# Performance work log

Hardware: AMD Instinct MI355X
Metric: run time of the kernel (lower is better)

## Reference

```python
import jax, jax.numpy as jnp
import numpy as np

TOPK = 6
E = 512
IN = 384
M = 8192
LN_EPS = 1e-5


def _lin(x, w, b):
    # torch nn.Linear: y = x @ W^T + b, W is [out, in]
    return x @ w.T + b


def setup_inputs() -> dict:
    key = jax.random.key(0)
    ks = jax.random.split(key, 16)
    s = lambda k, sh: (jax.random.normal(k, sh, dtype=jnp.float32) * 0.02)
    return {
        "x": jax.random.normal(ks[0], (1, M, IN), dtype=jnp.float32),
        "fc1_w": s(ks[1], (E, IN)), "fc1_b": jnp.zeros((E,), jnp.float32),
        "wh_w": s(ks[2], (E, E)),   "wh_b": jnp.zeros((E,), jnp.float32),
        "wt_w": s(ks[3], (E, E)),   "wt_b": jnp.zeros((E,), jnp.float32),
        "l1_w": s(ks[4], (E, E)),   "l1_b": jnp.zeros((E,), jnp.float32),
        "l2_w": s(ks[5], (E, E)),   "l2_b": jnp.zeros((E,), jnp.float32),
        "a1_w": s(ks[6], (E // 2, E)), "a1_b": jnp.zeros((E // 2,), jnp.float32),
        "a2_w": s(ks[7], (1, E // 2)), "a2_b": jnp.zeros((1,), jnp.float32),
        "ln_g": jnp.ones((E,), jnp.float32), "ln_b": jnp.zeros((E,), jnp.float32),
    }


def reference(x, fc1_w, fc1_b, wh_w, wh_b, wt_w, wt_b,
              l1_w, l1_b, l2_w, l2_b, a1_w, a1_b, a2_w, a2_b, ln_g, ln_b):
    lrelu = jax.nn.leaky_relu  # slope 0.01 == torch default
    h = lrelu(_lin(x, fc1_w, fc1_b))                      # [B,M,E]
    h = (h + h.mean(axis=1, keepdims=True)) * 0.5
    e_h = _lin(h, wh_w, wh_b)                             # [B,M,E]
    e_t = _lin(h, wt_w, wt_b)                             # [B,M,E]
    scale = E ** (-0.5)
    attn_logit = (e_h * scale) @ jnp.swapaxes(e_t, -2, -1)  # [B,M,M]
    topk_weight, topk_index = jax.lax.top_k(attn_logit, TOPK)  # [B,M,K]
    # gather top-k neighbor tail embeddings: [B,M,K,E]
    Nb_h = jax.vmap(lambda et, idx: et[idx])(e_t, topk_index)
    topk_prob = jax.nn.softmax(topk_weight, axis=2)       # [B,M,K]
    eh_r = topk_prob[..., None] * Nb_h + (1.0 - topk_prob)[..., None] * e_h[:, :, None, :]
    gate = jnp.tanh(e_h[:, :, None, :] + eh_r)            # [B,M,K,E]
    # faithful to torch einsum('ijkl,ijkm->ijk'): sums l and m independently
    ka_weight = Nb_h.sum(axis=-1) * gate.sum(axis=-1)     # [B,M,K]
    ka_prob = jax.nn.softmax(ka_weight, axis=2)           # [B,M,K]
    e_Nh = jnp.einsum('bmk,bmke->bme', ka_prob, Nb_h)     # [B,M,E]
    sum_emb = lrelu(_lin(e_h + e_Nh, l1_w, l1_b))
    bi_emb = lrelu(_lin(e_h * e_Nh, l2_w, l2_b))
    emb = sum_emb + bi_emb                                # [B,M,E] (dropout = eval identity)
    hn = emb[0]                                           # squeeze(0) -> [M,E]
    # GeoGlobalAttention readout: gate_nn = Linear->LeakyReLU->Linear, softmax over nodes
    g = _lin(lrelu(_lin(hn, a1_w, a1_b)), a2_w, a2_b)     # [M,1]
    att = jax.nn.softmax(g, axis=0)
    pooled = (att * hn).sum(axis=0, keepdims=True)        # [1,E]
    mu = pooled.mean(axis=-1, keepdims=True)
    var = jnp.mean((pooled - mu) ** 2, axis=-1, keepdims=True)
    out = (pooled - mu) / jnp.sqrt(var + LN_EPS) * ln_g + ln_b
    return out
```

## Files before the change

kernel.cpp:

```cpp
#include <hip/hip_runtime.h>
#include <math.h>
#include <stdint.h>

#define M_NODES 8192
#define E_DIM   512
#define NTOPK   6
#define ATTN_SCALE 0.04419417382415922f

typedef __attribute__((ext_vector_type(8))) short short8;
typedef __attribute__((ext_vector_type(4))) float f32x4;

__device__ __forceinline__ float lrelu(float v) { return v > 0.f ? v : 0.01f * v; }

__device__ __forceinline__ unsigned short f2bf(float f) {
  uint32_t u = __float_as_uint(f);
  uint32_t r = (u + 0x7FFFu + ((u >> 16) & 1u)) >> 16;
  return (unsigned short)r;
}
__device__ __forceinline__ float bf2f(unsigned short s) {
  return __uint_as_float(((uint32_t)s) << 16);
}

__device__ __forceinline__ void async_cp16(const void* gptr, void* lds) {
  auto g1 = reinterpret_cast<const __attribute__((address_space(1))) unsigned int*>(
      reinterpret_cast<uintptr_t>(gptr));
  auto l3 = reinterpret_cast<__attribute__((address_space(3))) unsigned int*>(
      reinterpret_cast<uintptr_t>(lds));
  __builtin_amdgcn_global_load_lds(g1, l3, 16, 0, 0);
}



__global__ __launch_bounds__(256) void wcast_kernel(
    const float* __restrict__ x, const float* __restrict__ fc1w,
    const float* __restrict__ whw, const float* __restrict__ wtw,
    const float* __restrict__ l1w, const float* __restrict__ l2w,
    const float* __restrict__ a1w,
    unsigned short* __restrict__ xT, unsigned short* __restrict__ fc1T,
    unsigned short* __restrict__ whT, unsigned short* __restrict__ wtT,
    unsigned short* __restrict__ l1T, unsigned short* __restrict__ l2T,
    unsigned short* __restrict__ a1T)
{
  const int gid = blockIdx.x * 256 + threadIdx.x;
  const float* src; unsigned short* dst; int K8, local;
  if (gid < 417792) {
    K8 = 48;
    if (gid < 393216) { src = x; dst = xT; local = gid; }
    else { src = fc1w; dst = fc1T; local = gid - 393216; }
  } else {
    K8 = 64;
    if (gid < 450560)      { src = whw; dst = whT; local = gid - 417792; }
    else if (gid < 483328) { src = wtw; dst = wtT; local = gid - 450560; }
    else if (gid < 516096) { src = l1w; dst = l1T; local = gid - 483328; }
    else if (gid < 548864) { src = l2w; dst = l2T; local = gid - 516096; }
    else                   { src = a1w; dst = a1T; local = gid - 548864; }
  }
  const int m = local / K8;
  const int k8 = local - m * K8;
  const float* p = src + (size_t)m * (K8 * 8) + k8 * 8;
  float4 v0 = ((const float4*)p)[0];
  float4 v1 = ((const float4*)p)[1];
  const int Kt = K8 >> 2;
  const size_t ti = ((size_t)(m >> 4) * Kt + (k8 >> 2)) * 512 + ((m & 15) + 16 * (k8 & 3)) * 8;
  uint4 pk;
  pk.x = (uint32_t)f2bf(v0.x) | ((uint32_t)f2bf(v0.y) << 16);
  pk.y = (uint32_t)f2bf(v0.z) | ((uint32_t)f2bf(v0.w) << 16);
  pk.z = (uint32_t)f2bf(v1.x) | ((uint32_t)f2bf(v1.y) << 16);
  pk.w = (uint32_t)f2bf(v1.z) | ((uint32_t)f2bf(v1.w) << 16);
  *(uint4*)(dst + ti) = pk;
}

__global__ __launch_bounds__(256, 4) void gemm1_kernel(
    const unsigned short* __restrict__ xT, const unsigned short* __restrict__ fc1T,
    const float* __restrict__ b1, unsigned short* __restrict__ hT,
    float* __restrict__ colsum)
{
  __shared__ unsigned short As[8 * 512];
  __shared__ unsigned short Bs[8 * 512];
  const int tid = threadIdx.x, lane = tid & 63, w = tid >> 6;
  const int wr = w >> 1, wc = w & 1;
  const int m0 = blockIdx.y * 128;
  const int n0 = blockIdx.x * 128;

  f32x4 acc[4][4];
#pragma unroll
  for (int i = 0; i < 4; i++)
#pragma unroll
    for (int j = 0; j < 4; j++) acc[i][j] = (f32x4){0.f, 0.f, 0.f, 0.f};

  for (int kt = 0; kt < 12; kt++) {
    const int s0 = w, s1 = w + 4;
    async_cp16(xT + ((size_t)((m0 >> 4) + s0) * 12 + kt) * 512 + lane * 8, &As[s0 * 512]);
    async_cp16(xT + ((size_t)((m0 >> 4) + s1) * 12 + kt) * 512 + lane * 8, &As[s1 * 512]);
    async_cp16(fc1T + ((size_t)((n0 >> 4) + s0) * 12 + kt) * 512 + lane * 8, &Bs[s0 * 512]);
    async_cp16(fc1T + ((size_t)((n0 >> 4) + s1) * 12 + kt) * 512 + lane * 8, &Bs[s1 * 512]);
    __syncthreads();
    short8 a[4], b[4];
#pragma unroll
    for (int i = 0; i < 4; i++) a[i] = *(const short8*)&As[(wr * 4 + i) * 512 + lane * 8];
#pragma unroll
    for (int j = 0; j < 4; j++) b[j] = *(const short8*)&Bs[(wc * 4 + j) * 512 + lane * 8];
#pragma unroll
    for (int i = 0; i < 4; i++)
#pragma unroll
      for (int j = 0; j < 4; j++)
        acc[i][j] = __builtin_amdgcn_mfma_f32_16x16x32_bf16(a[i], b[j], acc[i][j], 0, 0, 0);
    __syncthreads();
  }

  const int q = lane >> 4, lcol = lane & 15;
  float colp[4] = {};
#pragma unroll
  for (int i = 0; i < 4; i++)
#pragma unroll
    for (int j = 0; j < 4; j++) {
      const int c = n0 + wc * 64 + j * 16 + lcol;
      const float bias = b1[c];
#pragma unroll
      for (int d = 0; d < 4; d++) {
        const int r = m0 + wr * 64 + i * 16 + q * 4 + d;
        const float v = 0.5f * lrelu(acc[i][j][d] + bias);
        hT[((size_t)(r >> 4) * 16 + (c >> 5)) * 512 +
           ((r & 15) + 16 * ((c >> 3) & 3)) * 8 + (c & 7)] = f2bf(v);
        colp[j] += v;
      }
    }
#pragma unroll
  for (int j = 0; j < 4; j++) {
    colp[j] += __shfl_xor(colp[j], 16);
    colp[j] += __shfl_xor(colp[j], 32);
  }
  if (lane < 16) {
#pragma unroll
    for (int j = 0; j < 4; j++)
      atomicAdd(&colsum[n0 + wc * 64 + j * 16 + lcol], colp[j]);
  }
}

__global__ __launch_bounds__(256) void meanproj_kernel(
    const float* __restrict__ colsum, const float* __restrict__ whw,
    const float* __restrict__ wtw, const float* __restrict__ whb,
    const float* __restrict__ wtb, float* __restrict__ biasHT)
{
  const int lane = threadIdx.x & 63;
  const int c1024 = blockIdx.x * 4 + (threadIdx.x >> 6);
  const bool isH = c1024 < 512;
  const int c = isH ? c1024 : c1024 - 512;
  const float* W = (isH ? whw : wtw) + (size_t)c * 512 + lane * 8;
  const float* cs = colsum + lane * 8;
  float s = 0.f;
#pragma unroll
  for (int e = 0; e < 8; e++) s = fmaf(cs[e], W[e], s);
#pragma unroll
  for (int off = 32; off; off >>= 1) s += __shfl_xor(s, off);
  if (lane == 0)
    biasHT[c1024] = (isH ? whb : wtb)[c] + s * (1.f / (float)M_NODES);
}

__global__ __launch_bounds__(256, 4) void dual_gemm(
    const unsigned short* __restrict__ hT, const unsigned short* __restrict__ wstackT,
    const float* __restrict__ biasHT,
    unsigned short* __restrict__ ehT, unsigned short* __restrict__ etT,
    unsigned short* __restrict__ ehRow, unsigned short* __restrict__ etRow)
{
  __shared__ unsigned short As[8 * 512];
  __shared__ unsigned short Bs[8 * 512];
  const int tid = threadIdx.x, lane = tid & 63, w = tid >> 6;
  const int wr = w >> 1, wc = w & 1;
  const int m0 = blockIdx.y * 128;
  const int n0 = blockIdx.x * 128;

  f32x4 acc[4][4];
#pragma unroll
  for (int i = 0; i < 4; i++)
#pragma unroll
    for (int j = 0; j < 4; j++) acc[i][j] = (f32x4){0.f, 0.f, 0.f, 0.f};

  for (int kt = 0; kt < 16; kt++) {
    const int s0 = w, s1 = w + 4;
    async_cp16(hT + ((size_t)((m0 >> 4) + s0) * 16 + kt) * 512 + lane * 8, &As[s0 * 512]);
    async_cp16(hT + ((size_t)((m0 >> 4) + s1) * 16 + kt) * 512 + lane * 8, &As[s1 * 512]);
    async_cp16(wstackT + ((size_t)((n0 >> 4) + s0) * 16 + kt) * 512 + lane * 8, &Bs[s0 * 512]);
    async_cp16(wstackT + ((size_t)((n0 >> 4) + s1) * 16 + kt) * 512 + lane * 8, &Bs[s1 * 512]);
    __syncthreads();
    short8 a[4], b[4];
#pragma unroll
    for (int i = 0; i < 4; i++) a[i] = *(const short8*)&As[(wr * 4 + i) * 512 + lane * 8];
#pragma unroll
    for (int j = 0; j < 4; j++) b[j] = *(const short8*)&Bs[(wc * 4 + j) * 512 + lane * 8];
#pragma unroll
    for (int i = 0; i < 4; i++)
#pragma unroll
      for (int j = 0; j < 4; j++)
        acc[i][j] = __builtin_amdgcn_mfma_f32_16x16x32_bf16(a[i], b[j], acc[i][j], 0, 0, 0);
    __syncthreads();
  }

  const int q = lane >> 4, lcol = lane & 15;
  const bool isH = (n0 < 512);
  const int cb = isH ? n0 : (n0 - 512);
  unsigned short* T = isH ? ehT : etT;
  unsigned short* R = isH ? ehRow : etRow;

#pragma unroll
  for (int i = 0; i < 4; i++)
#pragma unroll
    for (int j = 0; j < 4; j++) {
      const int cl = wc * 64 + j * 16 + lcol;
      const float bias = biasHT[n0 + cl];
      const int c = cb + cl;
#pragma unroll
      for (int d = 0; d < 4; d++) {
        const int r = m0 + wr * 64 + i * 16 + q * 4 + d;
        const unsigned short us = f2bf(acc[i][j][d] + bias);
        T[((size_t)(r >> 4) * 16 + (c >> 5)) * 512 +
          ((r & 15) + 16 * ((c >> 3) & 3)) * 8 + (c & 7)] = us;
        R[(size_t)r * E_DIM + c] = us;
      }
    }
}

template <int MODE>
__global__ __launch_bounds__(256) void mfma_gemm(
    const unsigned short* __restrict__ At1, const unsigned short* __restrict__ At2,
    const unsigned short* __restrict__ Wt1, const unsigned short* __restrict__ Wt2,
    const float* __restrict__ b1, const float* __restrict__ b2,
    float* __restrict__ Cf, unsigned short* __restrict__ T1,
    unsigned short* __restrict__ Cbf, int N, int K)
{
  constexpr bool DUALW = (MODE == 2);
  __shared__ unsigned short As[2][8 * 512];
  __shared__ unsigned short Bs[2][4 * 512];
  const int Kt = K >> 5;
  const int tid = threadIdx.x, lane = tid & 63, w = tid >> 6;
  const int m0 = blockIdx.y * 128, n0 = blockIdx.x * 64;

  f32x4 acc0[2][4], acc1[2][4];
#pragma unroll
  for (int p = 0; p < 2; p++)
#pragma unroll
    for (int j = 0; j < 4; j++) {
      acc0[p][j] = (f32x4){0.f, 0.f, 0.f, 0.f};
      acc1[p][j] = (f32x4){0.f, 0.f, 0.f, 0.f};
    }

  for (int kt = 0; kt < Kt; kt++) {
    const unsigned short* a1p = At1 + ((size_t)((m0 >> 4) + 2 * w) * Kt + kt) * 512 + lane * 8;
    async_cp16(a1p, &As[0][(2 * w) * 512]);
    async_cp16(a1p + (size_t)Kt * 512, &As[0][(2 * w + 1) * 512]);
    if (MODE == 2) {
      const unsigned short* a2p = At2 + ((size_t)((m0 >> 4) + 2 * w) * Kt + kt) * 512 + lane * 8;
      async_cp16(a2p, &As[1][(2 * w) * 512]);
      async_cp16(a2p + (size_t)Kt * 512, &As[1][(2 * w + 1) * 512]);
    }
    const unsigned short* bp1 = Wt1 + ((size_t)((n0 >> 4) + w) * Kt + kt) * 512 + lane * 8;
    async_cp16(bp1, &Bs[0][w * 512]);
    if (DUALW) {
      const unsigned short* bp2 = Wt2 + ((size_t)((n0 >> 4) + w) * Kt + kt) * 512 + lane * 8;
      async_cp16(bp2, &Bs[1][w * 512]);
    }
    __syncthreads();
    short8 a[2], a2[2], bb[4], bb2[4];
#pragma unroll
    for (int p = 0; p < 2; p++) a[p] = *(const short8*)&As[0][(2 * w + p) * 512 + lane * 8];
    if (MODE == 2) {
#pragma unroll
      for (int p = 0; p < 2; p++) a2[p] = *(const short8*)&As[1][(2 * w + p) * 512 + lane * 8];
    }
#pragma unroll
    for (int j = 0; j < 4; j++) bb[j] = *(const short8*)&Bs[0][j * 512 + lane * 8];
    if (DUALW) {
#pragma unroll
      for (int j = 0; j < 4; j++) bb2[j] = *(const short8*)&Bs[1][j * 512 + lane * 8];
    }
#pragma unroll
    for (int p = 0; p < 2; p++)
#pragma unroll
      for (int j = 0; j < 4; j++) {
        acc0[p][j] = __builtin_amdgcn_mfma_f32_16x16x32_bf16(a[p], bb[j], acc0[p][j], 0, 0, 0);
        if (MODE == 2)
          acc1[p][j] = __builtin_amdgcn_mfma_f32_16x16x32_bf16(a2[p], bb2[j], acc1[p][j], 0, 0, 0);
      }
    __syncthreads();
  }

  const int lrow = (lane >> 4) * 4, lcol = lane & 15;

  if (MODE == 3) {
    float part[2][4] = {};
#pragma unroll
    for (int p = 0; p < 2; p++)
#pragma unroll
      for (int j = 0; j < 4; j++) {
        const int c = n0 + j * 16 + lcol;
        const float bias1 = b1[c];
        const float w2 = b2[c];
#pragma unroll
        for (int d = 0; d < 4; d++)
          part[p][d] = fmaf(lrelu(acc0[p][j][d] + bias1), w2, part[p][d]);
      }
#pragma unroll
    for (int p = 0; p < 2; p++)
#pragma unroll
      for (int d = 0; d < 4; d++) {
#pragma unroll
        for (int off = 1; off < 16; off <<= 1)
          part[p][d] += __shfl_xor(part[p][d], off);
      }
    if (lcol == 0) {
#pragma unroll
      for (int p = 0; p < 2; p++)
#pragma unroll
        for (int d = 0; d < 4; d++)
          atomicAdd(&Cf[m0 + w * 32 + p * 16 + lrow + d], part[p][d]);
    }
    return;
  }

  const int NT = N >> 5;
#pragma unroll
  for (int p = 0; p < 2; p++)
#pragma unroll
    for (int j = 0; j < 4; j++) {
      const int c = n0 + j * 16 + lcol;
      const float bias1 = b1[c];
      const float bias2 = b2[c];
#pragma unroll
      for (int d = 0; d < 4; d++) {
        const int r = m0 + w * 32 + p * 16 + lrow + d;
        const float e = lrelu(acc0[p][j][d] + bias1) + lrelu(acc1[p][j][d] + bias2);
        T1[((size_t)(r >> 4) * NT + (c >> 5)) * 512 +
           ((r & 15) + 16 * ((c >> 3) & 3)) * 8 + (c & 7)] = f2bf(e);
        Cbf[(size_t)r * N + c] = f2bf(e);
      }
    }
}

__global__ __launch_bounds__(256, 4) void sgemm_kernel(
    const unsigned short* __restrict__ ehT, const unsigned short* __restrict__ etT,
    uint32_t* __restrict__ cand)
{
  __shared__ unsigned short SH[128 * 130];
  unsigned short* As = SH;
  unsigned short* Bs = SH + 4096;
  const int tid = threadIdx.x, lane = tid & 63, w = tid >> 6;
  const int wr = w >> 1, wc = w & 1;
  const int m0 = blockIdx.y * 128;
  const int n0 = blockIdx.x * 128;

  f32x4 acc[4][4];
#pragma unroll
  for (int i = 0; i < 4; i++)
#pragma unroll
    for (int j = 0; j < 4; j++) acc[i][j] = (f32x4){0.f, 0.f, 0.f, 0.f};

  for (int kt = 0; kt < 16; kt++) {
    const int s0 = w, s1 = w + 4;
    async_cp16(ehT + ((size_t)((m0 >> 4) + s0) * 16 + kt) * 512 + lane * 8, &As[s0 * 512]);
    async_cp16(ehT + ((size_t)((m0 >> 4) + s1) * 16 + kt) * 512 + lane * 8, &As[s1 * 512]);
    async_cp16(etT + ((size_t)((n0 >> 4) + s0) * 16 + kt) * 512 + lane * 8, &Bs[s0 * 512]);
    async_cp16(etT + ((size_t)((n0 >> 4) + s1) * 16 + kt) * 512 + lane * 8, &Bs[s1 * 512]);
    __syncthreads();
    short8 a[4], b[4];
#pragma unroll
    for (int i = 0; i < 4; i++) a[i] = *(const short8*)&As[(wr * 4 + i) * 512 + lane * 8];
#pragma unroll
    for (int j = 0; j < 4; j++) b[j] = *(const short8*)&Bs[(wc * 4 + j) * 512 + lane * 8];
#pragma unroll
    for (int i = 0; i < 4; i++)
#pragma unroll
      for (int j = 0; j < 4; j++)
        acc[i][j] = __builtin_amdgcn_mfma_f32_16x16x32_bf16(a[i], b[j], acc[i][j], 0, 0, 0);
    __syncthreads();
  }

  const int q = lane >> 4, lcol = lane & 15;

#pragma unroll
  for (int i = 0; i < 4; i++)
#pragma unroll
    for (int j = 0; j < 4; j++) {
      const int colb = wc * 64 + j * 16 + lcol;
#pragma unroll
      for (int d = 0; d < 4; d++)
        SH[(wr * 64 + i * 16 + q * 4 + d) * 130 + colb] = f2bf(acc[i][j][d]);
    }
  __syncthreads();

  const int r = tid >> 1, half = tid & 1;
  const uint32_t* rowp = (const uint32_t*)SH + r * 65 + half * 32;
  const int cbase = n0 + half * 64;
  uint32_t t0 = 0, t1 = 0, t2 = 0, t3 = 0, t4 = 0, t5 = 0;
#pragma unroll 4
  for (int cc = 0; cc < 32; cc++) {
    const uint32_t v = rowp[cc];
#pragma unroll
    for (int e = 0; e < 2; e++) {
      const uint32_t h = e ? (v >> 16) : (v & 0xFFFFu);
      const uint32_t o16 = (h & 0x8000u) ? ((~h) & 0xFFFFu) : (h | 0x8000u);
      const uint32_t k = (o16 << 16) | (uint32_t)(8191 - (cbase + 2 * cc + e));
      if (k > t5) {
        t5 = k;
        uint32_t tmp;
        if (t5 > t4) { tmp = t4; t4 = t5; t5 = tmp; }
        if (t4 > t3) { tmp = t3; t3 = t4; t4 = tmp; }
        if (t3 > t2) { tmp = t2; t2 = t3; t3 = tmp; }
        if (t2 > t1) { tmp = t1; t1 = t2; t2 = tmp; }
        if (t1 > t0) { tmp = t0; t0 = t1; t1 = tmp; }
      }
    }
  }

  uint32_t b0 = (uint32_t)__shfl_xor((int)t0, 1);
  uint32_t b1 = (uint32_t)__shfl_xor((int)t1, 1);
  uint32_t b2 = (uint32_t)__shfl_xor((int)t2, 1);
  uint32_t b3 = (uint32_t)__shfl_xor((int)t3, 1);
  uint32_t b4 = (uint32_t)__shfl_xor((int)t4, 1);
  uint32_t b5 = (uint32_t)__shfl_xor((int)t5, 1);
  uint32_t wk[6];
#pragma unroll
  for (int t = 0; t < 6; t++) {
    if (t0 > b0) {
      wk[t] = t0;
      t0 = t1; t1 = t2; t2 = t3; t3 = t4; t4 = t5; t5 = 0u;
    } else {
      wk[t] = b0;
      b0 = b1; b1 = b2; b2 = b3; b3 = b4; b4 = b5; b5 = 0u;
    }
  }

  if (half == 0) {
    uint32_t* cp = cand + ((size_t)blockIdx.x * M_NODES + m0 + r) * 6;
    uint2 p01; p01.x = wk[0]; p01.y = wk[1];
    uint2 p23; p23.x = wk[2]; p23.y = wk[3];
    uint2 p45; p45.x = wk[4]; p45.y = wk[5];
    ((uint2*)cp)[0] = p01;
    ((uint2*)cp)[1] = p23;
    ((uint2*)cp)[2] = p45;
  }
}

__global__ __launch_bounds__(256) void combine_kernel(
    const uint32_t* __restrict__ cand,
    const unsigned short* __restrict__ ehRow, const unsigned short* __restrict__ etRow,
    unsigned short* __restrict__ s1T, unsigned short* __restrict__ s2T)
{
  const int tid = threadIdx.x;
  const int lane = tid & 63;
  const int w = tid >> 6;
  const int row = blockIdx.x * 4 + w;
  const int m = row;

  const uint32_t* cp = cand + ((size_t)lane * M_NODES + row) * 6;
  const uint2 v01 = ((const uint2*)cp)[0];
  const uint2 v23 = ((const uint2*)cp)[1];
  const uint2 v45 = ((const uint2*)cp)[2];
  uint32_t a0 = v01.x, a1 = v01.y, a2 = v23.x, a3 = v23.y, a4 = v45.x, a5 = v45.y;

  float wv[NTOPK]; int id[NTOPK];
#pragma unroll
  for (int t = 0; t < NTOPK; t++) {
    uint32_t mm = a0;
#pragma unroll
    for (int off = 1; off < 64; off <<= 1) {
      const uint32_t o = (uint32_t)__shfl_xor((int)mm, off);
      mm = mm > o ? mm : o;
    }
    if (a0 == mm) {
      a0 = a1; a1 = a2; a2 = a3; a3 = a4; a4 = a5; a5 = 0u;
    }
    const uint32_t h = mm >> 16;
    const uint32_t u = (h & 0x8000u) ? ((h & 0x7FFFu) << 16)
                                     : ((~h & 0xFFFFu) << 16);
    wv[t] = __uint_as_float(u) * ATTN_SCALE;
    id[t] = 8191 - (int)(mm & 0x1FFFu);
  }

  float mx = wv[0];
#pragma unroll
  for (int k = 1; k < NTOPK; k++) mx = fmaxf(mx, wv[k]);
  float p[NTOPK]; float s = 0.f;
#pragma unroll
  for (int k = 0; k < NTOPK; k++) { p[k] = expf(wv[k] - mx); s += p[k]; }
  const float inv = 1.f / s;
#pragma unroll
  for (int k = 0; k < NTOPK; k++) p[k] *= inv;

  short8 eh8 = *(const short8*)(ehRow + (size_t)m * E_DIM + lane * 8);
  float ehv[8];
#pragma unroll
  for (int e = 0; e < 8; e++) ehv[e] = bf2f((unsigned short)eh8[e]);

  float nv[NTOPK][8];
#pragma unroll
  for (int k = 0; k < NTOPK; k++) {
    short8 nb = *(const short8*)(etRow + (size_t)id[k] * E_DIM + lane * 8);
#pragma unroll
    for (int e = 0; e < 8; e++) nv[k][e] = bf2f((unsigned short)nb[e]);
  }

  float ka[NTOPK];
#pragma unroll
  for (int k = 0; k < NTOPK; k++) {
    float snb = 0.f, sg = 0.f;
    const float aa = 2.f - p[k], bb = p[k];
#pragma unroll
    for (int e = 0; e < 8; e++) {
      snb += nv[k][e];
      sg += tanhf(fmaf(aa, ehv[e], bb * nv[k][e]));
    }
#pragma unroll
    for (int off = 32; off; off >>= 1) {
      snb += __shfl_xor(snb, off);
      sg += __shfl_xor(sg, off);
    }
    ka[k] = snb * sg;
  }
  float km = ka[0];
#pragma unroll
  for (int k = 1; k < NTOPK; k++) km = fmaxf(km, ka[k]);
  float kp[NTOPK]; float ks = 0.f;
#pragma unroll
  for (int k = 0; k < NTOPK; k++) { kp[k] = expf(ka[k] - km); ks += kp[k]; }
  const float kinv = 1.f / ks;

  const size_t tbase = ((size_t)(m >> 4) * 16 + (lane >> 2)) * 512 +
                       ((m & 15) + 16 * (lane & 3)) * 8;
  unsigned short o1[8], o2[8];
#pragma unroll
  for (int e = 0; e < 8; e++) {
    float o = 0.f;
#pragma unroll
    for (int k = 0; k < NTOPK; k++) o = fmaf(kp[k], nv[k][e], o);
    o *= kinv;
    o1[e] = f2bf(ehv[e] + o);
    o2[e] = f2bf(ehv[e] * o);
  }
  *(short8*)(s1T + tbase) = *(short8*)o1;
  *(short8*)(s2T + tbase) = *(short8*)o2;
}

__global__ __launch_bounds__(256) void pooled_kernel(
    const unsigned short* __restrict__ emb, const float* __restrict__ g,
    float* __restrict__ pooled, float* __restrict__ wsum)
{
  const int t = threadIdx.x;
  const int r0 = blockIdx.x * 128;
  float a0 = 0.f, a1 = 0.f, lsum = 0.f;
  for (int r = 0; r < 128; r++) {
    const int m = r0 + r;
    const float wv = expf(g[m]);
    lsum += wv;
    a0 = fmaf(wv, bf2f(emb[(size_t)m * E_DIM + t]), a0);
    a1 = fmaf(wv, bf2f(emb[(size_t)m * E_DIM + 256 + t]), a1);
  }
  atomicAdd(&pooled[t], a0);
  atomicAdd(&pooled[t + 256], a1);
  if (t == 0) atomicAdd(wsum, lsum);
}

__global__ __launch_bounds__(512) void ln_kernel(
    const float* __restrict__ pooled, const float* __restrict__ wsum,
    const float* __restrict__ lng, const float* __restrict__ lnb,
    float* __restrict__ out)
{
  __shared__ float red[8];
  __shared__ float red2[8];
  const int t = threadIdx.x;
  const float v = pooled[t] / wsum[0];
  float s = v;
#pragma unroll
  for (int off = 32; off; off >>= 1) s += __shfl_xor(s, off);
  if ((t & 63) == 0) red[t >> 6] = s;
  __syncthreads();
  float tot = 0.f;
  for (int i = 0; i < 8; i++) tot += red[i];
  const float mu = tot / (float)E_DIM;
  const float d = v - mu;
  float q = d * d;
#pragma unroll
  for (int off = 32; off; off >>= 1) q += __shfl_xor(q, off);
  if ((t & 63) == 0) red2[t >> 6] = q;
  __syncthreads();
  float vt = 0.f;
  for (int i = 0; i < 8; i++) vt += red2[i];
  const float var = vt / (float)E_DIM;
  out[t] = d * rsqrtf(var + 1e-5f) * lng[t] + lnb[t];
}

extern "C" void kernel_launch(void* const* d_in, const int* in_sizes, int n_in,
                              void* d_out, int out_size, void* d_ws, size_t ws_size,
                              hipStream_t stream)
{
  const float* x     = (const float*)d_in[0];
  const float* fc1_w = (const float*)d_in[1];
  const float* fc1_b = (const float*)d_in[2];
  const float* wh_w  = (const float*)d_in[3];
  const float* wh_b  = (const float*)d_in[4];
  const float* wt_w  = (const float*)d_in[5];
  const float* wt_b  = (const float*)d_in[6];
  const float* l1_w  = (const float*)d_in[7];
  const float* l1_b  = (const float*)d_in[8];
  const float* l2_w  = (const float*)d_in[9];
  const float* l2_b  = (const float*)d_in[10];
  const float* a1_w  = (const float*)d_in[11];
  const float* a1_b  = (const float*)d_in[12];
  const float* a2_w  = (const float*)d_in[13];
  const float* a2_b  = (const float*)d_in[14];
  const float* ln_g  = (const float*)d_in[15];
  const float* ln_b  = (const float*)d_in[16];
  (void)a2_b;

  char* ws = (char*)d_ws;
  const size_t MiB = 1 << 20;
  unsigned short* fc1T = (unsigned short*)(ws + 0);
  unsigned short* whT  = (unsigned short*)(ws + 393216);
  unsigned short* wtT  = (unsigned short*)(ws + 917504);
  unsigned short* l1T  = (unsigned short*)(ws + 1441792);
  unsigned short* l2T  = (unsigned short*)(ws + 1966080);
  unsigned short* a1T  = (unsigned short*)(ws + 2490368);
  unsigned short* xT     = (unsigned short*)(ws + 3 * MiB);
  unsigned short* hT     = (unsigned short*)(ws + 25 * MiB);
  unsigned short* ehT    = (unsigned short*)(ws + 33 * MiB);
  unsigned short* etT    = (unsigned short*)(ws + 41 * MiB);
  unsigned short* ehRow  = (unsigned short*)(ws + 49 * MiB);
  unsigned short* etRow  = (unsigned short*)(ws + 57 * MiB);
  unsigned short* s1T    = (unsigned short*)(ws + 3 * MiB);
  unsigned short* s2T    = (unsigned short*)(ws + 11 * MiB);
  unsigned short* embT   = (unsigned short*)(ws + 19 * MiB);
  unsigned short* embRow = (unsigned short*)(ws + 27 * MiB);
  uint32_t*       cand   = (uint32_t*)(ws + 96 * MiB);
  char*           smal   = ws + 69 * MiB;
  float* colsum = (float*)(smal);
  float* biasHT = (float*)(smal + 2048);
  float* g      = (float*)(smal + 8192);
  float* stats  = (float*)(smal + 40960);
  float* pooled = (float*)(smal + 45056);

  hipMemsetAsync(smal, 0, 47104, stream);

  wcast_kernel<<<2208, 256, 0, stream>>>(x, fc1_w, wh_w, wt_w, l1_w, l2_w, a1_w,
                                         xT, fc1T, whT, wtT, l1T, l2T, a1T);
  gemm1_kernel<<<dim3(4, 64), 256, 0, stream>>>(xT, fc1T, fc1_b, hT, colsum);
  meanproj_kernel<<<256, 256, 0, stream>>>(colsum, wh_w, wt_w, wh_b, wt_b, biasHT);
  dual_gemm<<<dim3(8, 64), 256, 0, stream>>>(hT, whT, biasHT, ehT, etT, ehRow, etRow);
  sgemm_kernel<<<dim3(64, 64), 256, 0, stream>>>(ehT, etT, cand);
  combine_kernel<<<M_NODES / 4, 256, 0, stream>>>(cand, ehRow, etRow, s1T, s2T);
  mfma_gemm<2><<<dim3(8, 64), 256, 0, stream>>>(
      s1T, s2T, l1T, l2T, l1_b, l2_b, nullptr, embT, embRow, 512, 512);
  mfma_gemm<3><<<dim3(4, 64), 256, 0, stream>>>(
      embT, nullptr, a1T, nullptr, a1_b, a2_w, g, nullptr, nullptr, 256, 512);
  pooled_kernel<<<64, 256, 0, stream>>>(embRow, g, pooled, stats);
  ln_kernel<<<1, 512, 0, stream>>>(pooled, stats, ln_g, ln_b, (float*)d_out);
}
```

Before: 290.3 us.

## Drop row-major eh/et copies, read fragment layout in combine, speed top-k scan

The dual GEMM no longer writes separate row-major copies of e_h and e_t. The combine kernel instead gathers 8-element fragments straight from the MFMA-tiled transposed buffers, which removes half of that kernel's output writes. The similarity GEMM epilogue now packs bf16 pairs into 32-bit LDS stores in a permuted column order and remaps indices to match. Its top-k scan applies the order-preserving transform to both halves with one XOR and skips candidates early with a cheap 16-bit compare. Risks are strided gather patterns in combine and correctness of the permuted column mapping.

```diff
diff --git a/kernel.cpp b/kernel.cpp
--- a/kernel.cpp
+++ b/kernel.cpp
@@ -160,8 +160,7 @@
 __global__ __launch_bounds__(256, 4) void dual_gemm(
     const unsigned short* __restrict__ hT, const unsigned short* __restrict__ wstackT,
     const float* __restrict__ biasHT,
-    unsigned short* __restrict__ ehT, unsigned short* __restrict__ etT,
-    unsigned short* __restrict__ ehRow, unsigned short* __restrict__ etRow)
+    unsigned short* __restrict__ ehT, unsigned short* __restrict__ etT)
 {
   __shared__ unsigned short As[8 * 512];
   __shared__ unsigned short Bs[8 * 512];
@@ -200,7 +199,6 @@
   const bool isH = (n0 < 512);
   const int cb = isH ? n0 : (n0 - 512);
   unsigned short* T = isH ? ehT : etT;
-  unsigned short* R = isH ? ehRow : etRow;
 
 #pragma unroll
   for (int i = 0; i < 4; i++)
@@ -212,10 +210,8 @@
 #pragma unroll
       for (int d = 0; d < 4; d++) {
         const int r = m0 + wr * 64 + i * 16 + q * 4 + d;
-        const unsigned short us = f2bf(acc[i][j][d] + bias);
         T[((size_t)(r >> 4) * 16 + (c >> 5)) * 512 +
-          ((r & 15) + 16 * ((c >> 3) & 3)) * 8 + (c & 7)] = us;
-        R[(size_t)r * E_DIM + c] = us;
+          ((r & 15) + 16 * ((c >> 3) & 3)) * 8 + (c & 7)] = f2bf(acc[i][j][d] + bias);
       }
     }
 }
@@ -379,34 +375,40 @@
 #pragma unroll
   for (int i = 0; i < 4; i++)
 #pragma unroll
-    for (int j = 0; j < 4; j++) {
-      const int colb = wc * 64 + j * 16 + lcol;
-#pragma unroll
-      for (int d = 0; d < 4; d++)
-        SH[(wr * 64 + i * 16 + q * 4 + d) * 130 + colb] = f2bf(acc[i][j][d]);
+    for (int d = 0; d < 4; d++) {
+      const int rowb = wr * 64 + i * 16 + q * 4 + d;
+      const uint32_t p01 = (uint32_t)f2bf(acc[i][0][d]) | ((uint32_t)f2bf(acc[i][1][d]) << 16);
+      const uint32_t p23 = (uint32_t)f2bf(acc[i][2][d]) | ((uint32_t)f2bf(acc[i][3][d]) << 16);
+      uint32_t* wp = (uint32_t*)(SH + rowb * 130 + wc * 64 + lcol * 4);
+      wp[0] = p01;
+      wp[1] = p23;
     }
   __syncthreads();
 
   const int r = tid >> 1, half = tid & 1;
   const uint32_t* rowp = (const uint32_t*)SH + r * 65 + half * 32;
-  const int cbase = n0 + half * 64;
   uint32_t t0 = 0, t1 = 0, t2 = 0, t3 = 0, t4 = 0, t5 = 0;
-#pragma unroll 4
+#pragma unroll 8
   for (int cc = 0; cc < 32; cc++) {
     const uint32_t v = rowp[cc];
+    const uint32_t sgn = v & 0x80008000u;
+    const uint32_t ov = v ^ (0x80008000u | ((sgn >> 15) * 0x7FFFu));
 #pragma unroll
     for (int e = 0; e < 2; e++) {
-      const uint32_t h = e ? (v >> 16) : (v & 0xFFFFu);
-      const uint32_t o16 = (h & 0x8000u) ? ((~h) & 0xFFFFu) : (h | 0x8000u);
-      const uint32_t k = (o16 << 16) | (uint32_t)(8191 - (cbase + 2 * cc + e));
-      if (k > t5) {
-        t5 = k;
-        uint32_t tmp;
-        if (t5 > t4) { tmp = t4; t4 = t5; t5 = tmp; }
-        if (t4 > t3) { tmp = t3; t3 = t4; t4 = tmp; }
-        if (t3 > t2) { tmp = t2; t2 = t3; t3 = tmp; }
-        if (t2 > t1) { tmp = t1; t1 = t2; t2 = tmp; }
-        if (t1 > t0) { tmp = t0; t0 = t1; t1 = tmp; }
+      const uint32_t o16 = e ? (ov >> 16) : (ov & 0xFFFFu);
+      if (o16 >= (t5 >> 16)) {
+        const int cperm = half * 64 + cc * 2 + e;
+        const int col = n0 + (cperm >> 6) * 64 + (cperm & 3) * 16 + ((cperm >> 2) & 15);
+        const uint32_t k = (o16 << 16) | (uint32_t)(8191 - col);
+        if (k > t5) {
+          t5 = k;
+          uint32_t tmp;
+          if (t5 > t4) { tmp = t4; t4 = t5; t5 = tmp; }
+          if (t4 > t3) { tmp = t3; t3 = t4; t4 = tmp; }
+          if (t3 > t2) { tmp = t2; t2 = t3; t3 = tmp; }
+          if (t2 > t1) { tmp = t1; t1 = t2; t2 = tmp; }
+          if (t1 > t0) { tmp = t0; t0 = t1; t1 = tmp; }
+        }
       }
     }
   }
@@ -442,7 +444,7 @@
 
 __global__ __launch_bounds__(256) void combine_kernel(
     const uint32_t* __restrict__ cand,
-    const unsigned short* __restrict__ ehRow, const unsigned short* __restrict__ etRow,
+    const unsigned short* __restrict__ ehT, const unsigned short* __restrict__ etT,
     unsigned short* __restrict__ s1T, unsigned short* __restrict__ s2T)
 {
   const int tid = threadIdx.x;
@@ -450,6 +452,7 @@
   const int w = tid >> 6;
   const int row = blockIdx.x * 4 + w;
   const int m = row;
+  const size_t lfrag = (size_t)(lane >> 2) * 512 + 16 * (lane & 3) * 8;
 
   const uint32_t* cp = cand + ((size_t)lane * M_NODES + row) * 6;
   const uint2 v01 = ((const uint2*)cp)[0];
@@ -486,7 +489,7 @@
 #pragma unroll
   for (int k = 0; k < NTOPK; k++) p[k] *= inv;
 
-  short8 eh8 = *(const short8*)(ehRow + (size_t)m * E_DIM + lane * 8);
+  short8 eh8 = *(const short8*)&ehT[((size_t)(m >> 4) * 16) * 512 + (m & 15) * 8 + lfrag];
   float ehv[8];
 #pragma unroll
   for (int e = 0; e < 8; e++) ehv[e] = bf2f((unsigned short)eh8[e]);
@@ -494,7 +497,7 @@
   float nv[NTOPK][8];
 #pragma unroll
   for (int k = 0; k < NTOPK; k++) {
-    short8 nb = *(const short8*)(etRow + (size_t)id[k] * E_DIM + lane * 8);
+    short8 nb = *(const short8*)&etT[((size_t)(id[k] >> 4) * 16) * 512 + (id[k] & 15) * 8 + lfrag];
 #pragma unroll
     for (int e = 0; e < 8; e++) nv[k][e] = bf2f((unsigned short)nb[e]);
   }
@@ -623,8 +626,6 @@
   unsigned short* hT     = (unsigned short*)(ws + 25 * MiB);
   unsigned short* ehT    = (unsigned short*)(ws + 33 * MiB);
   unsigned short* etT    = (unsigned short*)(ws + 41 * MiB);
-  unsigned short* ehRow  = (unsigned short*)(ws + 49 * MiB);
-  unsigned short* etRow  = (unsigned short*)(ws + 57 * MiB);
   unsigned short* s1T    = (unsigned short*)(ws + 3 * MiB);
   unsigned short* s2T    = (unsigned short*)(ws + 11 * MiB);
   unsigned short* embT   = (unsigned short*)(ws + 19 * MiB);
@@ -643,9 +644,9 @@
                                          xT, fc1T, whT, wtT, l1T, l2T, a1T);
   gemm1_kernel<<<dim3(4, 64), 256, 0, stream>>>(xT, fc1T, fc1_b, hT, colsum);
   meanproj_kernel<<<256, 256, 0, stream>>>(colsum, wh_w, wt_w, wh_b, wt_b, biasHT);
-  dual_gemm<<<dim3(8, 64), 256, 0, stream>>>(hT, whT, biasHT, ehT, etT, ehRow, etRow);
+  dual_gemm<<<dim3(8, 64), 256, 0, stream>>>(hT, whT, biasHT, ehT, etT);
   sgemm_kernel<<<dim3(64, 64), 256, 0, stream>>>(ehT, etT, cand);
-  combine_kernel<<<M_NODES / 4, 256, 0, stream>>>(cand, ehRow, etRow, s1T, s2T);
+  combine_kernel<<<M_NODES / 4, 256, 0, stream>>>(cand, ehT, etT, s1T, s2T);
   mfma_gemm<2><<<dim3(8, 64), 256, 0, stream>>>(
       s1T, s2T, l1T, l2T, l1_b, l2_b, nullptr, embT, embRow, 512, 512);
   mfma_gemm<3><<<dim3(4, 64), 256, 0, stream>>>(
```

After: 299.7 us. 1.03x slower.
